# Performance work log

Hardware: AMD Instinct MI355X
Metric: run time of the kernel (lower is better)

Reference implementation:

```python
import jax, jax.numpy as jnp
import numpy as np

NUM_HEADS = 12

def setup_inputs() -> dict:
    key = jax.random.key(0)
    ks = jax.random.split(key, 6)
    B, N, C = 4, 2048, 768
    s = 0.02
    return {
        "x": jax.random.normal(ks[0], (B, N, C), jnp.float32),
        "y": jax.random.normal(ks[1], (B, N, C), jnp.float32),
        "Wq": jax.random.normal(ks[2], (C, C), jnp.float32) * s,
        "Wkv": jax.random.normal(ks[3], (2 * C, C), jnp.float32) * s,
        "tau_param": jnp.asarray(1.0, jnp.float32),
        "Wproj": jax.random.normal(ks[4], (C, C), jnp.float32) * s,
        "bproj": jnp.zeros((C,), jnp.float32),
    }

def reference(x, y, Wq, Wkv, tau_param, Wproj, bproj):
    B, N, C = x.shape
    H = NUM_HEADS
    D = C // H
    scale = D ** -0.5
    # q: [B,H,N,D]
    q = (x @ Wq.T).reshape(B, N, H, D).transpose(0, 2, 1, 3) * scale
    kv = (y @ Wkv.T).reshape(B, N, 2, H, D).transpose(2, 0, 3, 1, 4)
    k, v = kv[0], kv[1]
    tau = jax.nn.softplus(tau_param) + 1e-6
    attn = jnp.einsum("bhnd,bhmd->bhnm", q, k) / tau  # [B,H,N,N]
    attn = jax.nn.softmax(attn, axis=-1)
    out = jnp.einsum("bhnm,bhmd->bhnd", attn, v)  # [B,H,N,D]
    out = out.transpose(0, 2, 1, 3).reshape(B, N, C)
    return out @ Wproj.T + bproj
```

## Files before the change

### kernel.cpp

```cpp
#include <hip/hip_runtime.h>
#include <math.h>

typedef unsigned short u16;
typedef unsigned int u32;
typedef __fp16 fp16x2 __attribute__((ext_vector_type(2)));
typedef _Float16 half8 __attribute__((ext_vector_type(8)));
typedef float f32x4 __attribute__((ext_vector_type(4)));

#define NH   12
#define SEQ  2048
#define CDIM 768

__device__ __forceinline__ u16 f2h(float f) {
  _Float16 h = (_Float16)f;
  return __builtin_bit_cast(u16, h);
}
__device__ __forceinline__ u32 pk2(float a, float b) {
  fp16x2 h = __builtin_amdgcn_cvt_pkrtz(a, b);
  return __builtin_bit_cast(u32, h);
}
__device__ __forceinline__ void dma16(const u16* g, u16* l) {
  __builtin_amdgcn_global_load_lds(
      (const __attribute__((address_space(1))) u32*)g,
      (__attribute__((address_space(3))) u32*)l, 16, 0, 0);
}

__global__ __launch_bounds__(256) void cvt_xy(const float* __restrict__ x,
                                              const float* __restrict__ y,
                                              u16* __restrict__ xh, u16* __restrict__ yh) {
  const long NEL = 8192l * 768;
  long i = ((long)blockIdx.x * 256 + threadIdx.x) * 4;
  const float* in = (i < NEL) ? x : y;
  u16* out = (i < NEL) ? xh : yh;
  long j = (i < NEL) ? i : i - NEL;
  float4 f = *(const float4*)(in + j);
  *(uint2*)(out + j) = make_uint2(pk2(f.x, f.y), pk2(f.z, f.w));
}
__global__ __launch_bounds__(256) void cvt_w(const float* __restrict__ Wq,
                                             const float* __restrict__ Wkv,
                                             const float* __restrict__ Wp,
                                             const float* __restrict__ taup,
                                             u16* __restrict__ wqh, u16* __restrict__ wkh,
                                             u16* __restrict__ wph) {
  const long E1 = 768l * 768, E2 = E1 + 1536l * 768;
  long i = ((long)blockIdx.x * 256 + threadIdx.x) * 4;
  const float* in; u16* out; long j; float s;
  if (i < E1) {
    float t = *taup;
    float sp = (t > 20.f) ? t : log1pf(expf(t));
    s = (0.125f / (sp + 1e-6f)) * 1.44269504088896340736f;
    in = Wq; out = wqh; j = i;
  } else if (i < E2) {
    s = 1.f; in = Wkv; out = wkh; j = i - E1;
  } else {
    s = 1.f; in = Wp; out = wph; j = i - E2;
  }
  float4 f = *(const float4*)(in + j);
  *(uint2*)(out + j) = make_uint2(pk2(f.x * s, f.y * s), pk2(f.z * s, f.w * s));
}

template<int MODE>
__global__ __launch_bounds__(256, 3) void gemm_k(
    const u16* __restrict__ A0, const u16* __restrict__ A1,
    const u16* __restrict__ B0, const u16* __restrict__ B1,
    u16* __restrict__ oq, u16* __restrict__ ok, u16* __restrict__ ovt,
    float* __restrict__ outf, const float* __restrict__ bias)
{
  __shared__ __align__(16) u16 As[2][128 * 64];
  __shared__ __align__(16) u16 Bs[2][64 * 64];
  const int tid = threadIdx.x;
  const int wave = tid >> 6, lane = tid & 63;
  const int quad = lane >> 4, l16 = lane & 15;
  const int wr = wave >> 1, wc = wave & 1;
  const int row0 = blockIdx.x * 128;
  const int by = blockIdx.y;

  const u16* A; const u16* Bm; int cb;
  if (MODE == 0) {
    if (by < 12) { A = A0; Bm = B0; cb = by; }
    else         { A = A1; Bm = B1; cb = by - 12; }
  } else {
    A = A0; Bm = B0; cb = by;
  }
  const int col0 = cb * 64;

  const int sub = lane >> 3;
  const int csw = ((lane & 7) ^ sub) * 8;

  f32x4 acc[4][2] = {};

  auto stage = [&](int k0, int bsel) {
    #pragma unroll
    for (int i = 0; i < 4; i++) {
      int ii = wave * 4 + i;
      dma16(A + (size_t)(row0 + ii * 8 + sub) * 768 + k0 + csw, &As[bsel][ii * 512]);
    }
    #pragma unroll
    for (int i = 0; i < 2; i++) {
      int ii = wave * 2 + i;
      dma16(Bm + (size_t)(col0 + ii * 8 + sub) * 768 + k0 + csw, &Bs[bsel][ii * 512]);
    }
  };

  stage(0, 0);
  __syncthreads();

  #pragma unroll 1
  for (int t = 0; t < 12; t++) {
    const int cur = t & 1;
    if (t + 1 < 12) stage((t + 1) << 6, cur ^ 1);
    const u16* Asp = As[cur];
    const u16* Bsp = Bs[cur];
    #pragma unroll
    for (int ks = 0; ks < 2; ks++) {
      half8 af[4], bfr[2];
      #pragma unroll
      for (int mt = 0; mt < 4; mt++)
        af[mt] = *(const half8*)&Asp[(wr * 64 + mt * 16 + l16) * 64 + (((ks * 4 + quad) ^ (l16 & 7)) * 8)];
      #pragma unroll
      for (int nt = 0; nt < 2; nt++)
        bfr[nt] = *(const half8*)&Bsp[(wc * 32 + nt * 16 + l16) * 64 + (((ks * 4 + quad) ^ (l16 & 7)) * 8)];
      #pragma unroll
      for (int mt = 0; mt < 4; mt++)
        #pragma unroll
        for (int nt = 0; nt < 2; nt++)
          acc[mt][nt] = __builtin_amdgcn_mfma_f32_16x16x32_f16(af[mt], bfr[nt], acc[mt][nt], 0, 0, 0);
    }
    __syncthreads();
  }

  #pragma unroll
  for (int mt = 0; mt < 4; mt++)
  #pragma unroll
  for (int nt = 0; nt < 2; nt++) {
    int gm0 = row0 + wr * 64 + mt * 16 + quad * 4;
    int gn = col0 + wc * 32 + nt * 16 + l16;
    f32x4 v = acc[mt][nt];
    if (MODE == 0) {
      int b = gm0 >> 11, n0 = gm0 & 2047;
      if (by < 12) {
        int h = gn >> 6, d = gn & 63;
        size_t base = (((size_t)(b * NH + h)) * SEQ + n0) * 64 + d;
        #pragma unroll
        for (int r = 0; r < 4; r++) oq[base + (size_t)r * 64] = f2h(v[r]);
      } else if (gn < CDIM) {
        int h = gn >> 6, d = gn & 63;
        size_t base = (((size_t)(b * NH + h)) * SEQ + n0) * 64 + d;
        #pragma unroll
        for (int r = 0; r < 4; r++) ok[base + (size_t)r * 64] = f2h(v[r]);
      } else {
        int c = gn - CDIM;
        int h = c >> 6, d = c & 63;
        *(uint2*)&ovt[(((size_t)(b * NH + h)) * 64 + d) * SEQ + n0] =
            make_uint2(pk2(v[0], v[1]), pk2(v[2], v[3]));
      }
    } else {
      float bv = bias[gn];
      #pragma unroll
      for (int r = 0; r < 4; r++)
        outf[(size_t)(gm0 + r) * CDIM + gn] = v[r] + bv;
    }
  }
}

__global__ __launch_bounds__(256, 4) void attn_kernel(
    const u16* __restrict__ Q, const u16* __restrict__ Kb,
    const u16* __restrict__ Vtg, u16* __restrict__ Ob)
{
  __shared__ __align__(16) u16 Ks[2][64 * 64];
  __shared__ __align__(16) u16 Vs[2][64 * 64];
  __shared__ __align__(16) u16 Ps[4 * 16 * 64];

  const int bid = (blockIdx.x & 7) * 192 + (blockIdx.x >> 3);
  const int qt = bid & 31;
  const int bh = bid >> 5;
  const int b = bh / NH, h = bh % NH;
  const u16* Qp = Q   + (size_t)bh * SEQ * 64;
  const u16* Kp = Kb  + (size_t)bh * SEQ * 64;
  const u16* Vp = Vtg + (size_t)bh * 64 * SEQ;

  const int tid = threadIdx.x;
  const int wave = tid >> 6, lane = tid & 63;
  const int quad = lane >> 4, l16 = lane & 15;
  const int sub = lane >> 3;
  const int csw = ((lane & 7) ^ sub) * 8;
  u16* Pw = Ps + wave * 16 * 64;

  half8 vone;
  #pragma unroll
  for (int j = 0; j < 8; j++) vone[j] = (_Float16)1.0f;

  half8 qf[2];
  #pragma unroll
  for (int ks = 0; ks < 2; ks++)
    qf[ks] = *(const half8*)(Qp + (size_t)(qt * 64 + wave * 16 + l16) * 64 + ks * 32 + quad * 8);

  f32x4 oacc[4] = {};
  f32x4 lacc = {};

  auto stage = [&](int kt, int bsel) {
    #pragma unroll
    for (int i = 0; i < 2; i++) {
      int ii = wave * 2 + i;
      dma16(Kp + (size_t)(kt * 64 + ii * 8 + sub) * 64 + csw, &Ks[bsel][ii * 512]);
      dma16(Vp + (size_t)(ii * 8 + sub) * SEQ + kt * 64 + csw, &Vs[bsel][ii * 512]);
    }
  };

  stage(0, 0);
  __syncthreads();

  for (int kt = 0; kt < SEQ / 64; kt++) {
    const int cur = kt & 1;
    if (kt + 1 < SEQ / 64) stage(kt + 1, cur ^ 1);
    const u16* Ksp = Ks[cur];
    const u16* Vsp = Vs[cur];

    f32x4 sacc[4] = {};
    __builtin_amdgcn_s_setprio(1);
    #pragma unroll
    for (int ks = 0; ks < 2; ks++) {
      #pragma unroll
      for (int ntk = 0; ntk < 4; ntk++) {
        half8 kf = *(const half8*)&Ksp[(ntk * 16 + l16) * 64 + (((ks * 4 + quad) ^ (l16 & 7)) * 8)];
        sacc[ntk] = __builtin_amdgcn_mfma_f32_16x16x32_f16(kf, qf[ks], sacc[ntk], 0, 0, 0);
      }
    }
    __builtin_amdgcn_s_setprio(0);

    #pragma unroll
    for (int ntk = 0; ntk < 4; ntk++) {
      float p0 = __builtin_amdgcn_exp2f(sacc[ntk][0]);
      float p1 = __builtin_amdgcn_exp2f(sacc[ntk][1]);
      float p2 = __builtin_amdgcn_exp2f(sacc[ntk][2]);
      float p3 = __builtin_amdgcn_exp2f(sacc[ntk][3]);
      *(uint2*)&Pw[l16 * 64 + (((ntk * 2 + (quad >> 1)) ^ (l16 & 7)) * 8) + (quad & 1) * 4] =
          make_uint2(pk2(p0, p1), pk2(p2, p3));
    }
    half8 pf[2];
    #pragma unroll
    for (int ks = 0; ks < 2; ks++)
      pf[ks] = *(const half8*)&Pw[l16 * 64 + (((ks * 4 + quad) ^ (l16 & 7)) * 8)];

    __builtin_amdgcn_s_setprio(1);
    #pragma unroll
    for (int ks = 0; ks < 2; ks++) {
      #pragma unroll
      for (int dt = 0; dt < 4; dt++) {
        half8 vf = *(const half8*)&Vsp[(dt * 16 + l16) * 64 + (((ks * 4 + quad) ^ (l16 & 7)) * 8)];
        oacc[dt] = __builtin_amdgcn_mfma_f32_16x16x32_f16(pf[ks], vf, oacc[dt], 0, 0, 0);
      }
      lacc = __builtin_amdgcn_mfma_f32_16x16x32_f16(pf[ks], vone, lacc, 0, 0, 0);
    }
    __builtin_amdgcn_s_setprio(0);

    __syncthreads();
  }

  #pragma unroll
  for (int r = 0; r < 4; r++) {
    float inv = 1.0f / lacc[r];
    int n = qt * 64 + wave * 16 + quad * 4 + r;
    size_t base = ((size_t)b * SEQ + n) * CDIM + h * 64;
    #pragma unroll
    for (int dt = 0; dt < 4; dt++)
      Ob[base + dt * 16 + l16] = f2h(oacc[dt][r] * inv);
  }
}

extern "C" void kernel_launch(void* const* d_in, const int* in_sizes, int n_in,
                              void* d_out, int out_size, void* d_ws, size_t ws_size,
                              hipStream_t stream)
{
  const float* x     = (const float*)d_in[0];
  const float* y     = (const float*)d_in[1];
  const float* Wq    = (const float*)d_in[2];
  const float* Wkv   = (const float*)d_in[3];
  const float* taup  = (const float*)d_in[4];
  const float* Wproj = (const float*)d_in[5];
  const float* bproj = (const float*)d_in[6];
  float* out = (float*)d_out;

  char* ws = (char*)d_ws;
  size_t off = 0;
  auto alloc = [&](size_t bytes) { char* p = ws + off; off += bytes; return p; };
  u16* xh  = (u16*)alloc(8192ull * 768 * 2);
  u16* yh  = (u16*)alloc(8192ull * 768 * 2);
  u16* wqh = (u16*)alloc(768ull * 768 * 2);
  u16* wkh = (u16*)alloc(1536ull * 768 * 2);
  u16* wph = (u16*)alloc(768ull * 768 * 2);
  u16* qb  = (u16*)alloc(8192ull * 768 * 2);
  u16* kb  = (u16*)alloc(8192ull * 768 * 2);
  u16* vtb = (u16*)alloc(8192ull * 768 * 2);
  u16* ao  = (u16*)alloc(8192ull * 768 * 2);

  cvt_xy<<<12288, 256, 0, stream>>>(x, y, xh, yh);
  cvt_w<<<2304, 256, 0, stream>>>(Wq, Wkv, Wproj, taup, wqh, wkh, wph);

  gemm_k<0><<<dim3(64, 36), 256, 0, stream>>>(xh, yh, wqh, wkh, qb, kb, vtb, nullptr, nullptr);
  attn_kernel<<<dim3(1536), 256, 0, stream>>>(qb, kb, vtb, ao);
  gemm_k<2><<<dim3(64, 12), 256, 0, stream>>>(ao, nullptr, wph, nullptr, nullptr, nullptr, nullptr, out, bproj);
}
```

Measured before the change: 238.1 us.

## Enlarge attention query tile to 128 rows and widen QKV GEMM N-tile

The attention kernel now processes 128 query rows per block, 32 per wave as two 16-row subtiles, so each K/V tile staged in LDS is reused across twice as many queries. This halves the grid and the K/V traffic per query. The QKV projection GEMM moves to a 128-wide N tile with more accumulators per wave and lower occupancy bounds. The cost is higher register pressure, lower occupancy, and fewer blocks to spread across the CUs.

```diff
diff --git a/kernel.cpp b/kernel.cpp
--- a/kernel.cpp
+++ b/kernel.cpp
@@ -59,15 +59,16 @@
   *(uint2*)(out + j) = make_uint2(pk2(f.x * s, f.y * s), pk2(f.z * s, f.w * s));
 }
 
-template<int MODE>
-__global__ __launch_bounds__(256, 3) void gemm_k(
+template<int MODE, int BN, int WPB>
+__global__ __launch_bounds__(256, WPB) void gemm_k(
     const u16* __restrict__ A0, const u16* __restrict__ A1,
     const u16* __restrict__ B0, const u16* __restrict__ B1,
     u16* __restrict__ oq, u16* __restrict__ ok, u16* __restrict__ ovt,
     float* __restrict__ outf, const float* __restrict__ bias)
 {
+  constexpr int NT = BN / 32;
   __shared__ __align__(16) u16 As[2][128 * 64];
-  __shared__ __align__(16) u16 Bs[2][64 * 64];
+  __shared__ __align__(16) u16 Bs[2][BN * 64];
   const int tid = threadIdx.x;
   const int wave = tid >> 6, lane = tid & 63;
   const int quad = lane >> 4, l16 = lane & 15;
@@ -77,17 +78,17 @@
 
   const u16* A; const u16* Bm; int cb;
   if (MODE == 0) {
-    if (by < 12) { A = A0; Bm = B0; cb = by; }
-    else         { A = A1; Bm = B1; cb = by - 12; }
+    if (by < 6) { A = A0; Bm = B0; cb = by; }
+    else        { A = A1; Bm = B1; cb = by - 6; }
   } else {
     A = A0; Bm = B0; cb = by;
   }
-  const int col0 = cb * 64;
+  const int col0 = cb * BN;
 
   const int sub = lane >> 3;
   const int csw = ((lane & 7) ^ sub) * 8;
 
-  f32x4 acc[4][2] = {};
+  f32x4 acc[4][NT] = {};
 
   auto stage = [&](int k0, int bsel) {
     #pragma unroll
@@ -96,8 +97,8 @@
       dma16(A + (size_t)(row0 + ii * 8 + sub) * 768 + k0 + csw, &As[bsel][ii * 512]);
     }
     #pragma unroll
-    for (int i = 0; i < 2; i++) {
-      int ii = wave * 2 + i;
+    for (int i = 0; i < BN / 32; i++) {
+      int ii = wave * (BN / 32) + i;
       dma16(Bm + (size_t)(col0 + ii * 8 + sub) * 768 + k0 + csw, &Bs[bsel][ii * 512]);
     }
   };
@@ -113,17 +114,17 @@
     const u16* Bsp = Bs[cur];
     #pragma unroll
     for (int ks = 0; ks < 2; ks++) {
-      half8 af[4], bfr[2];
+      half8 af[4], bfr[NT];
       #pragma unroll
       for (int mt = 0; mt < 4; mt++)
         af[mt] = *(const half8*)&Asp[(wr * 64 + mt * 16 + l16) * 64 + (((ks * 4 + quad) ^ (l16 & 7)) * 8)];
       #pragma unroll
-      for (int nt = 0; nt < 2; nt++)
-        bfr[nt] = *(const half8*)&Bsp[(wc * 32 + nt * 16 + l16) * 64 + (((ks * 4 + quad) ^ (l16 & 7)) * 8)];
+      for (int nt = 0; nt < NT; nt++)
+        bfr[nt] = *(const half8*)&Bsp[(wc * (BN / 2) + nt * 16 + l16) * 64 + (((ks * 4 + quad) ^ (l16 & 7)) * 8)];
       #pragma unroll
       for (int mt = 0; mt < 4; mt++)
         #pragma unroll
-        for (int nt = 0; nt < 2; nt++)
+        for (int nt = 0; nt < NT; nt++)
           acc[mt][nt] = __builtin_amdgcn_mfma_f32_16x16x32_f16(af[mt], bfr[nt], acc[mt][nt], 0, 0, 0);
     }
     __syncthreads();
@@ -132,13 +133,13 @@
   #pragma unroll
   for (int mt = 0; mt < 4; mt++)
   #pragma unroll
-  for (int nt = 0; nt < 2; nt++) {
+  for (int nt = 0; nt < NT; nt++) {
     int gm0 = row0 + wr * 64 + mt * 16 + quad * 4;
-    int gn = col0 + wc * 32 + nt * 16 + l16;
+    int gn = col0 + wc * (BN / 2) + nt * 16 + l16;
     f32x4 v = acc[mt][nt];
     if (MODE == 0) {
       int b = gm0 >> 11, n0 = gm0 & 2047;
-      if (by < 12) {
+      if (by < 6) {
         int h = gn >> 6, d = gn & 63;
         size_t base = (((size_t)(b * NH + h)) * SEQ + n0) * 64 + d;
         #pragma unroll
@@ -163,7 +164,7 @@
   }
 }
 
-__global__ __launch_bounds__(256, 4) void attn_kernel(
+__global__ __launch_bounds__(256, 3) void attn_kernel(
     const u16* __restrict__ Q, const u16* __restrict__ Kb,
     const u16* __restrict__ Vtg, u16* __restrict__ Ob)
 {
@@ -171,9 +172,9 @@
   __shared__ __align__(16) u16 Vs[2][64 * 64];
   __shared__ __align__(16) u16 Ps[4 * 16 * 64];
 
-  const int bid = (blockIdx.x & 7) * 192 + (blockIdx.x >> 3);
-  const int qt = bid & 31;
-  const int bh = bid >> 5;
+  const int bid = (blockIdx.x & 7) * 96 + (blockIdx.x >> 3);
+  const int qt = bid & 15;
+  const int bh = bid >> 4;
   const int b = bh / NH, h = bh % NH;
   const u16* Qp = Q   + (size_t)bh * SEQ * 64;
   const u16* Kp = Kb  + (size_t)bh * SEQ * 64;
@@ -190,13 +191,15 @@
   #pragma unroll
   for (int j = 0; j < 8; j++) vone[j] = (_Float16)1.0f;
 
-  half8 qf[2];
-  #pragma unroll
-  for (int ks = 0; ks < 2; ks++)
-    qf[ks] = *(const half8*)(Qp + (size_t)(qt * 64 + wave * 16 + l16) * 64 + ks * 32 + quad * 8);
-
-  f32x4 oacc[4] = {};
-  f32x4 lacc = {};
+  half8 qf[2][2];
+  #pragma unroll
+  for (int mt = 0; mt < 2; mt++)
+    #pragma unroll
+    for (int ks = 0; ks < 2; ks++)
+      qf[mt][ks] = *(const half8*)(Qp + (size_t)(qt * 128 + wave * 32 + mt * 16 + l16) * 64 + ks * 32 + quad * 8);
+
+  f32x4 oacc[2][4] = {};
+  f32x4 lacc[2] = {};
 
   auto stage = [&](int kt, int bsel) {
     #pragma unroll
@@ -216,31 +219,35 @@
     const u16* Ksp = Ks[cur];
     const u16* Vsp = Vs[cur];
 
-    f32x4 sacc[4] = {};
+    f32x4 sacc[2][4] = {};
     __builtin_amdgcn_s_setprio(1);
     #pragma unroll
     for (int ks = 0; ks < 2; ks++) {
       #pragma unroll
       for (int ntk = 0; ntk < 4; ntk++) {
         half8 kf = *(const half8*)&Ksp[(ntk * 16 + l16) * 64 + (((ks * 4 + quad) ^ (l16 & 7)) * 8)];
-        sacc[ntk] = __builtin_amdgcn_mfma_f32_16x16x32_f16(kf, qf[ks], sacc[ntk], 0, 0, 0);
+        #pragma unroll
+        for (int mt = 0; mt < 2; mt++)
+          sacc[mt][ntk] = __builtin_amdgcn_mfma_f32_16x16x32_f16(kf, qf[mt][ks], sacc[mt][ntk], 0, 0, 0);
       }
     }
     __builtin_amdgcn_s_setprio(0);
 
-    #pragma unroll
-    for (int ntk = 0; ntk < 4; ntk++) {
-      float p0 = __builtin_amdgcn_exp2f(sacc[ntk][0]);
-      float p1 = __builtin_amdgcn_exp2f(sacc[ntk][1]);
-      float p2 = __builtin_amdgcn_exp2f(sacc[ntk][2]);
-      float p3 = __builtin_amdgcn_exp2f(sacc[ntk][3]);
-      *(uint2*)&Pw[l16 * 64 + (((ntk * 2 + (quad >> 1)) ^ (l16 & 7)) * 8) + (quad & 1) * 4] =
-          make_uint2(pk2(p0, p1), pk2(p2, p3));
-    }
-    half8 pf[2];
-    #pragma unroll
-    for (int ks = 0; ks < 2; ks++)
-      pf[ks] = *(const half8*)&Pw[l16 * 64 + (((ks * 4 + quad) ^ (l16 & 7)) * 8)];
+    half8 pf[2][2];
+    #pragma unroll
+    for (int mt = 0; mt < 2; mt++) {
+      #pragma unroll
+      for (int ntk = 0; ntk < 4; ntk++) {
+        float p0 = __builtin_amdgcn_exp2f(sacc[mt][ntk][0]);
+        float p1 = __builtin_amdgcn_exp2f(sacc[mt][ntk][1]);
+        float p2 = __builtin_amdgcn_exp2f(sacc[mt][ntk][2]);
+        float p3 = __builtin_amdgcn_exp2f(sacc[mt][ntk][3]);
+        *(uint2*)&Pw[l16 * 64 + (((ntk * 2 + (quad >> 1)) ^ (l16 & 7)) * 8) + (quad & 1) * 4] =
+            make_uint2(pk2(p0, p1), pk2(p2, p3));
+      }
+      pf[mt][0] = *(const half8*)&Pw[l16 * 64 + ((quad ^ (l16 & 7)) * 8)];
+      pf[mt][1] = *(const half8*)&Pw[l16 * 64 + (((4 + quad) ^ (l16 & 7)) * 8)];
+    }
 
     __builtin_amdgcn_s_setprio(1);
     #pragma unroll
@@ -248,9 +255,13 @@
       #pragma unroll
       for (int dt = 0; dt < 4; dt++) {
         half8 vf = *(const half8*)&Vsp[(dt * 16 + l16) * 64 + (((ks * 4 + quad) ^ (l16 & 7)) * 8)];
-        oacc[dt] = __builtin_amdgcn_mfma_f32_16x16x32_f16(pf[ks], vf, oacc[dt], 0, 0, 0);
+        #pragma unroll
+        for (int mt = 0; mt < 2; mt++)
+          oacc[mt][dt] = __builtin_amdgcn_mfma_f32_16x16x32_f16(pf[mt][ks], vf, oacc[mt][dt], 0, 0, 0);
       }
-      lacc = __builtin_amdgcn_mfma_f32_16x16x32_f16(pf[ks], vone, lacc, 0, 0, 0);
+      #pragma unroll
+      for (int mt = 0; mt < 2; mt++)
+        lacc[mt] = __builtin_amdgcn_mfma_f32_16x16x32_f16(pf[mt][ks], vone, lacc[mt], 0, 0, 0);
     }
     __builtin_amdgcn_s_setprio(0);
 
@@ -258,13 +269,16 @@
   }
 
   #pragma unroll
-  for (int r = 0; r < 4; r++) {
-    float inv = 1.0f / lacc[r];
-    int n = qt * 64 + wave * 16 + quad * 4 + r;
-    size_t base = ((size_t)b * SEQ + n) * CDIM + h * 64;
-    #pragma unroll
-    for (int dt = 0; dt < 4; dt++)
-      Ob[base + dt * 16 + l16] = f2h(oacc[dt][r] * inv);
+  for (int mt = 0; mt < 2; mt++) {
+    #pragma unroll
+    for (int r = 0; r < 4; r++) {
+      float inv = 1.0f / lacc[mt][r];
+      int n = qt * 128 + wave * 32 + mt * 16 + quad * 4 + r;
+      size_t base = ((size_t)b * SEQ + n) * CDIM + h * 64;
+      #pragma unroll
+      for (int dt = 0; dt < 4; dt++)
+        Ob[base + dt * 16 + l16] = f2h(oacc[mt][dt][r] * inv);
+    }
   }
 }
 
@@ -297,7 +311,7 @@
   cvt_xy<<<12288, 256, 0, stream>>>(x, y, xh, yh);
   cvt_w<<<2304, 256, 0, stream>>>(Wq, Wkv, Wproj, taup, wqh, wkh, wph);
 
-  gemm_k<0><<<dim3(64, 36), 256, 0, stream>>>(xh, yh, wqh, wkh, qb, kb, vtb, nullptr, nullptr);
-  attn_kernel<<<dim3(1536), 256, 0, stream>>>(qb, kb, vtb, ao);
-  gemm_k<2><<<dim3(64, 12), 256, 0, stream>>>(ao, nullptr, wph, nullptr, nullptr, nullptr, nullptr, out, bproj);
-}
+  gemm_k<0, 128, 2><<<dim3(64, 18), 256, 0, stream>>>(xh, yh, wqh, wkh, qb, kb, vtb, nullptr, nullptr);
+  attn_kernel<<<dim3(768), 256, 0, stream>>>(qb, kb, vtb, ao);
+  gemm_k<2, 64, 3><<<dim3(64, 12), 256, 0, stream>>>(ao, nullptr, wph, nullptr, nullptr, nullptr, nullptr, out, bproj);
+}
```

After: 230.0 us. 1.04x faster.
